# Kernel tuning notes

Hardware: AMD Instinct MI355X
Metric: run time of the kernel (lower is better)

## Reference

```python
import jax, jax.numpy as jnp
import numpy as np

LEN_M = 131328   # (data_dim+1) * d_h = 513 * 256
D_H = 256
N_MC = 64
DATA_DIM_P1 = 513
N = 4096


def setup_inputs() -> dict:
    key = jax.random.key(0)
    k1, k2, k3, k4 = jax.random.split(key, 4)
    params = jax.random.normal(k1, (2 * LEN_M,), dtype=jnp.float32)
    W1 = jax.random.normal(k2, (D_H + 1,), dtype=jnp.float32)
    x = jax.random.normal(k3, (N, DATA_DIM_P1), dtype=jnp.float32)
    eps = jax.random.normal(k4, (N_MC,), dtype=jnp.float32)
    return {"params": params, "W1": W1, "x": x, "eps": eps}


def reference(params, W1, x, eps):
    # split variational params into means and (relu'd) variances
    m_w0 = params[:LEN_M]                                  # [len_m]
    v_w0 = jax.nn.relu(params[LEN_M:]) + 1e-6              # [len_m]
    # reparameterized MC sampling; NOTE: torch code draws ONE scalar eps per
    # MC sample (randn(m_w0[0].shape) is scalar), shared across all weights.
    samps_w0 = m_w0[:, None] + eps[None, :] * jnp.sqrt(v_w0)[:, None]  # [len_m, M]
    W0 = samps_w0.reshape(DATA_DIM_P1, D_H, N_MC)          # [d+1, h, M]
    # fused batched GEMM replacing the d_h * num_MC_samps tiny matmuls
    x_w0 = jnp.einsum('nd,dhm->nhm', x, W0)                # [N, h, M]
    z = jax.nn.relu(x_w0)
    ones = jnp.ones((x.shape[0], 1, N_MC), dtype=x.dtype)
    z = jnp.concatenate([ones, z], axis=1)                 # [N, h+1, M]
    pred_samps = jnp.einsum('nhm,h->nm', z, W1)            # [N, M]
    return pred_samps, m_w0, v_w0
```

## Files before the change

kernel.cpp:

```cpp
#include <hip/hip_runtime.h>
#include <hip/hip_bf16.h>
#include <math.h>

#define LEN_M   131328
#define D_P1    513
#define NROW    4096
#define PRED_ELEMS (NROW * 64)

typedef __attribute__((ext_vector_type(8))) short short8;
typedef __attribute__((ext_vector_type(4))) float floatx4;
typedef __attribute__((ext_vector_type(2))) float v2f;

__device__ __forceinline__ void gl_lds16(const void* g, void* l)
{
    __builtin_amdgcn_global_load_lds(
        (const __attribute__((address_space(1))) unsigned int*)g,
        (__attribute__((address_space(3))) unsigned int*)l, 16, 0, 0);
}

__device__ __forceinline__ unsigned short bf16b(float f)
{
    __hip_bfloat16 h = __float2bfloat16(f);
    return *(unsigned short*)&h;
}

__global__ __launch_bounds__(256) void prep_kernel(
    const float* __restrict__ params, float* __restrict__ out,
    __hip_bfloat16* __restrict__ wcbt)
{
    __shared__ unsigned short T[64][65];
    const int bid = blockIdx.x;
    const int t   = threadIdx.x;

    if (bid < 513) {
        int i = bid * 256 + t;
        float m = params[i];
        float v = fmaxf(params[LEN_M + i], 0.0f) + 1e-6f;
        out[PRED_ELEMS + i]         = m;
        out[PRED_ELEMS + LEN_M + i] = v;
        return;
    }

    const int b2 = bid - 513;
    const int k0 = (b2 & 7) * 64;
    const int c0 = (b2 >> 3) * 64;
    const int hh = t & 63, kb = t >> 6;
    const bool spart = (c0 >= 256);
    const int hbase = c0 & 255;
    const float* src = params + (spart ? LEN_M : 0);

    #pragma unroll 4
    for (int p = 0; p < 16; ++p) {
        int kk = p * 4 + kb;
        float v = src[(k0 + kk) * 256 + hbase + hh];
        if (spart) v = sqrtf(fmaxf(v, 0.0f) + 1e-6f);
        T[kk][hh] = bf16b(v);
    }
    __syncthreads();

    const int cc = t >> 2, kq = t & 3;
    short8 lo, hi;
    #pragma unroll
    for (int j = 0; j < 8; ++j) lo[j] = (short)T[kq * 16 + j][cc];
    #pragma unroll
    for (int j = 0; j < 8; ++j) hi[j] = (short)T[kq * 16 + 8 + j][cc];

    const int cR = c0 + cc;
    const int g1 = (k0 >> 3) + 2 * kq;
    const int g2 = g1 + 1;
    const int d1 = (g1 >> 3) * 4096 + cR * 8 + ((g1 & 7) ^ (cR & 7));
    const int d2 = (g2 >> 3) * 4096 + cR * 8 + ((g2 & 7) ^ (cR & 7));
    short* wb = (short*)wcbt;
    *(short8*)(wb + d1 * 8) = lo;
    *(short8*)(wb + d2 * 8) = hi;
}

__global__ __launch_bounds__(512) void main_kernel(
    const __hip_bfloat16* __restrict__ wcbt, const float* __restrict__ params,
    const float* __restrict__ x, const float* __restrict__ W1,
    const float* __restrict__ eps, float* __restrict__ out)
{
    extern __shared__ char smem[];
    char*  Ap = smem + 131072;
    float* Cl = (float*)smem;
    float* P  = (float*)(smem + 40960);

    const int t = threadIdx.x;
    const int w = t >> 6, lane = t & 63;
    const int lane15 = lane & 15, quad = lane >> 4;
    const int ax7 = lane15 & 7;
    const int bm = blockIdx.x * 16;

    const char* wbase = (const char*)wcbt;

    #pragma unroll
    for (int i = 0; i < 8; ++i)
        gl_lds16(wbase + (0 * 4096 + i * 512 + t) * 16, smem + i * 8192 + t * 16);

    {
        const int r = t >> 5, seg = t & 31;
        const float* xrow = x + (bm + r) * D_P1 + seg * 16;
        #pragma unroll
        for (int c2 = 0; c2 < 2; ++c2) {
            int g  = seg * 2 + c2;
            int cs = (g & ~7) | ((g & 7) ^ (r & 7));
            short8 pk;
            #pragma unroll
            for (int j = 0; j < 8; ++j) pk[j] = (short)bf16b(xrow[c2 * 8 + j]);
            *(short8*)(Ap + r * 1024 + cs * 16) = pk;
        }
    }

    const float e = eps[lane];
    float xl[4];
    #pragma unroll
    for (int i = 0; i < 4; ++i)
        xl[i] = x[(bm + quad * 4 + i) * D_P1 + 512];
    float wl[4];
    #pragma unroll
    for (int s = 0; s < 4; ++s) {
        int c = (s < 2 ? 0 : 256) + w * 32 + (s & 1) * 16 + lane15;
        wl[s] = (c < 256) ? params[131072 + c]
                          : sqrtf(fmaxf(params[LEN_M + 131072 + (c - 256)], 0.0f) + 1e-6f);
    }

    int cb[4];
    #pragma unroll
    for (int s = 0; s < 4; ++s)
        cb[s] = ((s < 2 ? 0 : 256) + w * 32 + (s & 1) * 16 + lane15) * 128;

    floatx4 acc[4];
    #pragma unroll
    for (int s = 0; s < 4; ++s) acc[s] = (floatx4){0.f, 0.f, 0.f, 0.f};

    __syncthreads();

    for (int kc = 0; kc < 8; ++kc) {
        if (kc < 7) {
            const int nb = (kc + 1) & 1;
            #pragma unroll
            for (int i = 0; i < 8; ++i)
                gl_lds16(wbase + ((kc + 1) * 4096 + i * 512 + t) * 16,
                         smem + nb * 65536 + i * 8192 + t * 16);
        }
        const char* Bb = smem + (kc & 1) * 65536;
        const char* Ab = Ap + lane15 * 1024 + kc * 128;
        #pragma unroll
        for (int kk = 0; kk < 2; ++kk) {
            const int off = ((kk * 4 + quad) ^ ax7) * 16;
            short8 a  = *(const short8*)(Ab + off);
            short8 b0 = *(const short8*)(Bb + cb[0] + off);
            short8 b1 = *(const short8*)(Bb + cb[1] + off);
            short8 b2 = *(const short8*)(Bb + cb[2] + off);
            short8 b3 = *(const short8*)(Bb + cb[3] + off);
            acc[0] = __builtin_amdgcn_mfma_f32_16x16x32_bf16(a, b0, acc[0], 0, 0, 0);
            acc[1] = __builtin_amdgcn_mfma_f32_16x16x32_bf16(a, b1, acc[1], 0, 0, 0);
            acc[2] = __builtin_amdgcn_mfma_f32_16x16x32_bf16(a, b2, acc[2], 0, 0, 0);
            acc[3] = __builtin_amdgcn_mfma_f32_16x16x32_bf16(a, b3, acc[3], 0, 0, 0);
        }
        __syncthreads();
    }

    #pragma unroll
    for (int s = 0; s < 4; ++s) {
        int gc = (s < 2 ? 0 : 256) + w * 32 + (s & 1) * 16 + lane15;
        float4 o;
        o.x = acc[s][0] + xl[0] * wl[s];
        o.y = acc[s][1] + xl[1] * wl[s];
        o.z = acc[s][2] + xl[2] * wl[s];
        o.w = acc[s][3] + xl[3] * wl[s];
        *(float4*)&Cl[gc * 20 + quad * 4] = o;
    }
    __syncthreads();

    const int rq = (w & 3) * 4;
    const int hb = (w >> 2) * 128;
    v2f a01s = {0.f, 0.f}, a23s = {0.f, 0.f};
    const v2f e2 = {e, e}, z2 = {0.f, 0.f};

    #pragma unroll 4
    for (int hh = 0; hh < 128; ++hh) {
        const int h = hb + hh;
        const float w1h = W1[1 + h];
        const v2f w2 = {w1h, w1h};
        const float4 av = *(const float4*)&Cl[h * 20 + rq];
        const float4 bv = *(const float4*)&Cl[(256 + h) * 20 + rq];
        v2f a01 = {av.x, av.y}, a23 = {av.z, av.w};
        v2f b01 = {bv.x, bv.y}, b23 = {bv.z, bv.w};
        v2f t01 = __builtin_elementwise_max(__builtin_elementwise_fma(e2, b01, a01), z2);
        v2f t23 = __builtin_elementwise_max(__builtin_elementwise_fma(e2, b23, a23), z2);
        a01s = __builtin_elementwise_fma(t01, w2, a01s);
        a23s = __builtin_elementwise_fma(t23, w2, a23s);
    }

    if (w >= 4) {
        float* p = P + (w - 4) * 256 + lane;
        p[0]   = a01s.x; p[64]  = a01s.y;
        p[128] = a23s.x; p[192] = a23s.y;
    }
    __syncthreads();
    if (w < 4) {
        const float b0 = W1[0];
        const float* p = P + w * 256 + lane;
        float* op = out + (bm + rq) * 64 + lane;
        op[0]   = a01s.x + p[0]   + b0;
        op[64]  = a01s.y + p[64]  + b0;
        op[128] = a23s.x + p[128] + b0;
        op[192] = a23s.y + p[192] + b0;
    }
}

extern "C" void kernel_launch(void* const* d_in, const int* in_sizes, int n_in,
                              void* d_out, int out_size, void* d_ws, size_t ws_size,
                              hipStream_t stream)
{
    const float* params = (const float*)d_in[0];
    const float* W1     = (const float*)d_in[1];
    const float* x      = (const float*)d_in[2];
    const float* eps    = (const float*)d_in[3];
    float* out = (float*)d_out;
    __hip_bfloat16* wcbt = (__hip_bfloat16*)d_ws;

    static bool attr_set = false;
    if (!attr_set) {
        hipFuncSetAttribute((const void*)main_kernel,
                            hipFuncAttributeMaxDynamicSharedMemorySize, 147456);
        attr_set = true;
    }

    prep_kernel<<<513 + 64, 256, 0, stream>>>(params, out, wcbt);
    main_kernel<<<256, 512, 147456, stream>>>(wcbt, params, x, W1, eps, out);
}
```

Baseline: 84.43 us.

## Split hidden dimension across two blocks per row tile with atomic accumulation

```diff
diff --git a/kernel.cpp b/kernel.cpp
--- a/kernel.cpp
+++ b/kernel.cpp
@@ -40,8 +40,14 @@
         out[PRED_ELEMS + LEN_M + i] = v;
         return;
     }
-
-    const int b2 = bid - 513;
+    if (bid < 769) {
+        int i = (bid - 513) * 1024 + t * 4;
+        float4 z = {0.f, 0.f, 0.f, 0.f};
+        *(float4*)(out + i) = z;
+        return;
+    }
+
+    const int b2 = bid - 769;
     const int k0 = (b2 & 7) * 64;
     const int c0 = (b2 >> 3) * 64;
     const int hh = t & 63, kb = t >> 6;
@@ -81,21 +87,25 @@
     const float* __restrict__ eps, float* __restrict__ out)
 {
     extern __shared__ char smem[];
-    char*  Ap = smem + 131072;
+    char*  Ap = smem + 65536;
     float* Cl = (float*)smem;
-    float* P  = (float*)(smem + 40960);
 
     const int t = threadIdx.x;
     const int w = t >> 6, lane = t & 63;
     const int lane15 = lane & 15, quad = lane >> 4;
     const int ax7 = lane15 & 7;
-    const int bm = blockIdx.x * 16;
+    const int half = blockIdx.x & 1;
+    const int bm   = (blockIdx.x >> 1) * 16;
+    const int hoff8 = half * 1024;
 
     const char* wbase = (const char*)wcbt;
 
     #pragma unroll
-    for (int i = 0; i < 8; ++i)
-        gl_lds16(wbase + (0 * 4096 + i * 512 + t) * 16, smem + i * 8192 + t * 16);
+    for (int i = 0; i < 4; ++i) {
+        int j = i * 512 + t;
+        int src = hoff8 + j + (j & 1024);
+        gl_lds16(wbase + src * 16, smem + j * 16);
+    }
 
     {
         const int r = t >> 5, seg = t & 31;
@@ -116,98 +126,79 @@
     #pragma unroll
     for (int i = 0; i < 4; ++i)
         xl[i] = x[(bm + quad * 4 + i) * D_P1 + 512];
-    float wl[4];
-    #pragma unroll
-    for (int s = 0; s < 4; ++s) {
-        int c = (s < 2 ? 0 : 256) + w * 32 + (s & 1) * 16 + lane15;
-        wl[s] = (c < 256) ? params[131072 + c]
-                          : sqrtf(fmaxf(params[LEN_M + 131072 + (c - 256)], 0.0f) + 1e-6f);
-    }
-
-    int cb[4];
-    #pragma unroll
-    for (int s = 0; s < 4; ++s)
-        cb[s] = ((s < 2 ? 0 : 256) + w * 32 + (s & 1) * 16 + lane15) * 128;
-
-    floatx4 acc[4];
-    #pragma unroll
-    for (int s = 0; s < 4; ++s) acc[s] = (floatx4){0.f, 0.f, 0.f, 0.f};
+    int   lc[2];  float wl[2];
+    #pragma unroll
+    for (int s = 0; s < 2; ++s) {
+        lc[s] = w * 32 + s * 16 + lane15;
+        int gc = half * 128 + lc[s] + (lc[s] & 128);
+        wl[s] = (gc < 256) ? params[131072 + gc]
+                           : sqrtf(fmaxf(params[LEN_M + 131072 + (gc - 256)], 0.0f) + 1e-6f);
+    }
+    const int cb0 = lc[0] * 128, cb1 = lc[1] * 128;
+
+    floatx4 acc0 = {0.f,0.f,0.f,0.f}, acc1 = acc0;
 
     __syncthreads();
 
     for (int kc = 0; kc < 8; ++kc) {
         if (kc < 7) {
-            const int nb = (kc + 1) & 1;
+            char* nbuf = smem + ((kc + 1) & 1) * 32768;
             #pragma unroll
-            for (int i = 0; i < 8; ++i)
-                gl_lds16(wbase + ((kc + 1) * 4096 + i * 512 + t) * 16,
-                         smem + nb * 65536 + i * 8192 + t * 16);
-        }
-        const char* Bb = smem + (kc & 1) * 65536;
+            for (int i = 0; i < 4; ++i) {
+                int j = i * 512 + t;
+                int src = (kc + 1) * 4096 + hoff8 + j + (j & 1024);
+                gl_lds16(wbase + src * 16, nbuf + j * 16);
+            }
+        }
+        const char* Bb = smem + (kc & 1) * 32768;
         const char* Ab = Ap + lane15 * 1024 + kc * 128;
         #pragma unroll
         for (int kk = 0; kk < 2; ++kk) {
             const int off = ((kk * 4 + quad) ^ ax7) * 16;
             short8 a  = *(const short8*)(Ab + off);
-            short8 b0 = *(const short8*)(Bb + cb[0] + off);
-            short8 b1 = *(const short8*)(Bb + cb[1] + off);
-            short8 b2 = *(const short8*)(Bb + cb[2] + off);
-            short8 b3 = *(const short8*)(Bb + cb[3] + off);
-            acc[0] = __builtin_amdgcn_mfma_f32_16x16x32_bf16(a, b0, acc[0], 0, 0, 0);
-            acc[1] = __builtin_amdgcn_mfma_f32_16x16x32_bf16(a, b1, acc[1], 0, 0, 0);
-            acc[2] = __builtin_amdgcn_mfma_f32_16x16x32_bf16(a, b2, acc[2], 0, 0, 0);
-            acc[3] = __builtin_amdgcn_mfma_f32_16x16x32_bf16(a, b3, acc[3], 0, 0, 0);
+            short8 b0 = *(const short8*)(Bb + cb0 + off);
+            short8 b1 = *(const short8*)(Bb + cb1 + off);
+            acc0 = __builtin_amdgcn_mfma_f32_16x16x32_bf16(a, b0, acc0, 0, 0, 0);
+            acc1 = __builtin_amdgcn_mfma_f32_16x16x32_bf16(a, b1, acc1, 0, 0, 0);
         }
         __syncthreads();
     }
 
-    #pragma unroll
-    for (int s = 0; s < 4; ++s) {
-        int gc = (s < 2 ? 0 : 256) + w * 32 + (s & 1) * 16 + lane15;
-        float4 o;
-        o.x = acc[s][0] + xl[0] * wl[s];
-        o.y = acc[s][1] + xl[1] * wl[s];
-        o.z = acc[s][2] + xl[2] * wl[s];
-        o.w = acc[s][3] + xl[3] * wl[s];
-        *(float4*)&Cl[gc * 20 + quad * 4] = o;
+    {
+        floatx4 accs[2] = {acc0, acc1};
+        #pragma unroll
+        for (int s = 0; s < 2; ++s) {
+            float4 o;
+            o.x = accs[s][0] + xl[0] * wl[s];
+            o.y = accs[s][1] + xl[1] * wl[s];
+            o.z = accs[s][2] + xl[2] * wl[s];
+            o.w = accs[s][3] + xl[3] * wl[s];
+            *(float4*)&Cl[lc[s] * 20 + quad * 4] = o;
+        }
     }
     __syncthreads();
 
-    const int rq = (w & 3) * 4;
-    const int hb = (w >> 2) * 128;
-    v2f a01s = {0.f, 0.f}, a23s = {0.f, 0.f};
+    const int rq = w * 2;
+    v2f accp = {0.f, 0.f};
     const v2f e2 = {e, e}, z2 = {0.f, 0.f};
 
-    #pragma unroll 4
+    #pragma unroll 8
     for (int hh = 0; hh < 128; ++hh) {
-        const int h = hb + hh;
-        const float w1h = W1[1 + h];
+        const float w1h = W1[1 + half * 128 + hh];
         const v2f w2 = {w1h, w1h};
-        const float4 av = *(const float4*)&Cl[h * 20 + rq];
-        const float4 bv = *(const float4*)&Cl[(256 + h) * 20 + rq];
-        v2f a01 = {av.x, av.y}, a23 = {av.z, av.w};
-        v2f b01 = {bv.x, bv.y}, b23 = {bv.z, bv.w};
-        v2f t01 = __builtin_elementwise_max(__builtin_elementwise_fma(e2, b01, a01), z2);
-        v2f t23 = __builtin_elementwise_max(__builtin_elementwise_fma(e2, b23, a23), z2);
-        a01s = __builtin_elementwise_fma(t01, w2, a01s);
-        a23s = __builtin_elementwise_fma(t23, w2, a23s);
-    }
-
-    if (w >= 4) {
-        float* p = P + (w - 4) * 256 + lane;
-        p[0]   = a01s.x; p[64]  = a01s.y;
-        p[128] = a23s.x; p[192] = a23s.y;
-    }
-    __syncthreads();
-    if (w < 4) {
+        const v2f av = *(const v2f*)&Cl[hh * 20 + rq];
+        const v2f bv = *(const v2f*)&Cl[(128 + hh) * 20 + rq];
+        v2f tt = __builtin_elementwise_max(__builtin_elementwise_fma(e2, bv, av), z2);
+        accp = __builtin_elementwise_fma(tt, w2, accp);
+    }
+    if (half == 0) {
         const float b0 = W1[0];
-        const float* p = P + w * 256 + lane;
-        float* op = out + (bm + rq) * 64 + lane;
-        op[0]   = a01s.x + p[0]   + b0;
-        op[64]  = a01s.y + p[64]  + b0;
-        op[128] = a23s.x + p[128] + b0;
-        op[192] = a23s.y + p[192] + b0;
-    }
+        accp.x += b0; accp.y += b0;
+    }
+
+    float* op = out + (bm + rq) * 64 + lane;
+    unsafeAtomicAdd(op,      accp.x);
+    unsafeAtomicAdd(op + 64, accp.y);
 }
 
 extern "C" void kernel_launch(void* const* d_in, const int* in_sizes, int n_in,
@@ -224,10 +215,10 @@
     static bool attr_set = false;
     if (!attr_set) {
         hipFuncSetAttribute((const void*)main_kernel,
-                            hipFuncAttributeMaxDynamicSharedMemorySize, 147456);
+                            hipFuncAttributeMaxDynamicSharedMemorySize, 81920);
         attr_set = true;
     }
 
-    prep_kernel<<<513 + 64, 256, 0, stream>>>(params, out, wcbt);
-    main_kernel<<<256, 512, 147456, stream>>>(wcbt, params, x, W1, eps, out);
-}
+    prep_kernel<<<833, 256, 0, stream>>>(params, out, wcbt);
+    main_kernel<<<512, 512, 81920, stream>>>(wcbt, params, x, W1, eps, out);
+}
```

Result: no change. 84.53 us (+0.1%).
